# Kernel optimization log

Measured on AMD Instinct MI355X. Metric: run time of the kernel, lower is better.

## Reference

```python
import jax, jax.numpy as jnp
import numpy as np

B, S, D = 2, 1024, 1024
N_HEADS = 16
R = 128
M = 8
N_NEURONS = 256


def group_gate(gate, n_basis):
    # gate: [B,S,N] -> [B,S,M], sum over consecutive groups, then normalize
    b, s, n = gate.shape
    gs = n // n_basis  # exact by construction (256/8)
    g = gate.reshape(b, s, n_basis, gs).sum(axis=-1)
    return g / (g.sum(axis=-1, keepdims=True) + 1e-8)


def feature_fn(x, neurons, weights):
    # x:[B,S,D], neurons:[M,D,R], weights:[B,S,M] -> h:[B,S,R]
    all_h = jnp.einsum('bsd,mdr->bsmr', x, neurons)
    return jnp.einsum('bsmr,bsm->bsr', all_h, weights)


def restore_fn(h, neurons, weights):
    # h:[B,S,R], neurons:[M,R,D], weights:[B,S,M] -> [B,S,D]
    pre = jnp.einsum('bsr,bsm->bsmr', h, weights)
    return jnp.einsum('bsmr,mrd->bsd', pre, neurons)


def setup_inputs() -> dict:
    key = jax.random.key(0)
    ks = jax.random.split(key, 9)
    sc = 0.02
    return {
        'x': jax.random.normal(ks[0], (B, S, D), jnp.float32),
        'qk_f': jax.random.normal(ks[1], (M, D, R), jnp.float32) * sc,
        'qk_r': jax.random.normal(ks[2], (M, R, D), jnp.float32) * sc,
        'v_f': jax.random.normal(ks[3], (M, D, R), jnp.float32) * sc,
        'v_r': jax.random.normal(ks[4], (M, R, D), jnp.float32) * sc,
        'Wg_q': jax.random.normal(ks[5], (D, N_NEURONS), jnp.float32) * sc,
        'Wg_k': jax.random.normal(ks[6], (D, N_NEURONS), jnp.float32) * sc,
        'Wg_v': jax.random.normal(ks[7], (D, N_NEURONS), jnp.float32) * sc,
        'W_O': jax.random.normal(ks[8], (D, D), jnp.float32) * sc,
    }


def reference(x, qk_f, qk_r, v_f, v_r, Wg_q, Wg_k, Wg_v, W_O):
    # Router gates (softmax over neuron dim), then grouped per basis
    g_Q = jax.nn.softmax(jnp.einsum('bsd,dn->bsn', x, Wg_q), axis=-1)
    g_K = jax.nn.softmax(jnp.einsum('bsd,dn->bsn', x, Wg_k), axis=-1)
    g_V = jax.nn.softmax(jnp.einsum('bsd,dn->bsn', x, Wg_v), axis=-1)
    gQ_b = group_gate(g_Q, M)
    gK_b = group_gate(g_K, M)
    gV_b = group_gate(g_V, M)

    Q = restore_fn(feature_fn(x, qk_f, gQ_b), qk_r, gQ_b)
    K = restore_fn(feature_fn(x, qk_f, gK_b), qk_r, gK_b)
    V = restore_fn(feature_fn(x, v_f, gV_b), v_r, gV_b)

    d_head = D // N_HEADS
    Q = Q.reshape(B, S, N_HEADS, d_head).transpose(0, 2, 1, 3)
    K = K.reshape(B, S, N_HEADS, d_head).transpose(0, 2, 1, 3)
    V = V.reshape(B, S, N_HEADS, d_head).transpose(0, 2, 1, 3)

    scale = jnp.sqrt(jnp.float32(d_head))
    scores = jnp.einsum('bhsd,bhtd->bhst', Q, K) / scale
    causal = jnp.tril(jnp.ones((S, S), dtype=jnp.bool_))
    scores = jnp.where(causal, scores, jnp.finfo(scores.dtype).min)
    attn_w = jax.nn.softmax(scores, axis=-1)
    out = jnp.einsum('bhst,bhtd->bhsd', attn_w, V)
    out = out.transpose(0, 2, 1, 3).reshape(B, S, D)
    out = jnp.einsum('bsd,de->bse', out, W_O)
    return out
```

## Files before the change

### kernel.cpp

```cpp
#include <hip/hip_runtime.h>
#include <hip/hip_bf16.h>

#define BB 2
#define SS 1024
#define DD 1024
#define NH 16
#define DH 64
#define MM 8
#define RR 128
#define NN 256
#define NT (BB*SS)

using bf16 = __hip_bfloat16;

typedef __attribute__((ext_vector_type(8))) short short8;
typedef __attribute__((ext_vector_type(4))) short short4v;
typedef __attribute__((ext_vector_type(4))) float f32x4;

#define EXP2F(x) __builtin_amdgcn_exp2f(x)

#define GLD16(g, l) __builtin_amdgcn_global_load_lds( \
    (const __attribute__((address_space(1))) void*)(g), \
    (__attribute__((address_space(3))) void*)(l), 16, 0, 0)

__device__ __forceinline__ short8 lds_load8(const short* p) {
    short4v a = *(const short4v*)p;
    short4v b = *(const short4v*)(p + 4);
    short8 r;
    r[0] = a[0]; r[1] = a[1]; r[2] = a[2]; r[3] = a[3];
    r[4] = b[0]; r[5] = b[1]; r[6] = b[2]; r[7] = b[3];
    return r;
}

template <int NR>
__device__ __forceinline__ void stage_tile(const bf16* __restrict__ src, int k0,
                                           bf16* lds, int wave, int lane) {
#pragma unroll
    for (int i = 0; i < NR / 32; ++i) {
        const int L = i * 256 + wave * 64 + lane;
        const int row = L >> 3;
        const int gch = (L & 7) ^ ((row >> 1) & 7);
        GLD16(src + (size_t)row * DD + k0 + gch * 8, &lds[(i * 256 + wave * 64) * 8]);
    }
}

__device__ __forceinline__ short8 fragld(const bf16* lds, int rc, int kk, int quad) {
    int slot = (kk * 4 + quad) ^ ((rc >> 1) & 7);
    return *(const short8*)&((const short*)lds)[(rc * 8 + slot) * 8];
}

__device__ __forceinline__ void gemm64_std(
    const bf16* __restrict__ A, const bf16* __restrict__ Bt, bf16* __restrict__ C,
    int Nz, int m0, int n0, bf16* As, bf16* Bs,
    int wave, int lane, int quad, int l15) {
    const int wr = wave >> 1, wc = wave & 1;
    f32x4 acc[2][4];
#pragma unroll
    for (int i = 0; i < 2; ++i)
#pragma unroll
        for (int j = 0; j < 4; ++j) acc[i][j] = (f32x4)0.f;

    const bf16* Ab = A + (size_t)m0 * DD;
    const bf16* Bb = Bt + (size_t)n0 * DD;
    for (int k0 = 0; k0 < DD; k0 += 64) {
        __syncthreads();
        stage_tile<64>(Ab, k0, As, wave, lane);
        stage_tile<128>(Bb, k0, Bs, wave, lane);
        __syncthreads();
#pragma unroll
        for (int kk = 0; kk < 2; ++kk) {
            short8 aF[2], bF[4];
#pragma unroll
            for (int bi = 0; bi < 2; ++bi) aF[bi] = fragld(As, wr * 32 + bi * 16 + l15, kk, quad);
#pragma unroll
            for (int bj = 0; bj < 4; ++bj) bF[bj] = fragld(Bs, wc * 64 + bj * 16 + l15, kk, quad);
#pragma unroll
            for (int bi = 0; bi < 2; ++bi)
#pragma unroll
                for (int bj = 0; bj < 4; ++bj)
                    acc[bi][bj] = __builtin_amdgcn_mfma_f32_16x16x32_bf16(aF[bi], bF[bj], acc[bi][bj], 0, 0, 0);
        }
    }
#pragma unroll
    for (int bi = 0; bi < 2; ++bi)
#pragma unroll
        for (int bj = 0; bj < 4; ++bj)
#pragma unroll
            for (int r = 0; r < 4; ++r) {
                int row = m0 + wr * 32 + bi * 16 + quad * 4 + r;
                int col = n0 + wc * 64 + bj * 16 + l15;
                C[(size_t)row * Nz + col] = __float2bfloat16(acc[bi][bj][r]);
            }
}

__device__ __forceinline__ void gemm64_dualB(
    const bf16* __restrict__ A, const bf16* __restrict__ B0, const bf16* __restrict__ B1,
    bf16* __restrict__ C0, bf16* __restrict__ C1,
    int m0, int n0, bf16* As, bf16* Bs0, bf16* Bs1,
    int wave, int lane, int quad, int l15) {
    const int wr = wave >> 1, wc = wave & 1;
    f32x4 acc0[2][4], acc1[2][4];
#pragma unroll
    for (int i = 0; i < 2; ++i)
#pragma unroll
        for (int j = 0; j < 4; ++j) { acc0[i][j] = (f32x4)0.f; acc1[i][j] = (f32x4)0.f; }

    const bf16* Ab  = A  + (size_t)m0 * DD;
    const bf16* B0b = B0 + (size_t)n0 * DD;
    const bf16* B1b = B1 + (size_t)n0 * DD;
    for (int k0 = 0; k0 < DD; k0 += 64) {
        __syncthreads();
        stage_tile<64>(Ab, k0, As, wave, lane);
        stage_tile<128>(B0b, k0, Bs0, wave, lane);
        stage_tile<128>(B1b, k0, Bs1, wave, lane);
        __syncthreads();
#pragma unroll
        for (int kk = 0; kk < 2; ++kk) {
            short8 aF[2], bF[4];
#pragma unroll
            for (int bi = 0; bi < 2; ++bi) aF[bi] = fragld(As, wr * 32 + bi * 16 + l15, kk, quad);
#pragma unroll
            for (int bj = 0; bj < 4; ++bj) bF[bj] = fragld(Bs0, wc * 64 + bj * 16 + l15, kk, quad);
#pragma unroll
            for (int bi = 0; bi < 2; ++bi)
#pragma unroll
                for (int bj = 0; bj < 4; ++bj)
                    acc0[bi][bj] = __builtin_amdgcn_mfma_f32_16x16x32_bf16(aF[bi], bF[bj], acc0[bi][bj], 0, 0, 0);
#pragma unroll
            for (int bj = 0; bj < 4; ++bj) bF[bj] = fragld(Bs1, wc * 64 + bj * 16 + l15, kk, quad);
#pragma unroll
            for (int bi = 0; bi < 2; ++bi)
#pragma unroll
                for (int bj = 0; bj < 4; ++bj)
                    acc1[bi][bj] = __builtin_amdgcn_mfma_f32_16x16x32_bf16(aF[bi], bF[bj], acc1[bi][bj], 0, 0, 0);
        }
    }
#pragma unroll
    for (int bi = 0; bi < 2; ++bi)
#pragma unroll
        for (int bj = 0; bj < 4; ++bj)
#pragma unroll
            for (int r = 0; r < 4; ++r) {
                int row = m0 + wr * 32 + bi * 16 + quad * 4 + r;
                int col = n0 + wc * 64 + bj * 16 + l15;
                C0[(size_t)row * DD + col] = __float2bfloat16(acc0[bi][bj][r]);
                C1[(size_t)row * DD + col] = __float2bfloat16(acc1[bi][bj][r]);
            }
}

__device__ __forceinline__ void gemm64_dualA(
    const bf16* __restrict__ A0, const bf16* __restrict__ A1, const bf16* __restrict__ Bt,
    bf16* __restrict__ C0, bf16* __restrict__ C1,
    int m0, int n0, bf16* As0, bf16* As1, bf16* Bs,
    int wave, int lane, int quad, int l15) {
    const int wr = wave >> 1, wc = wave & 1;
    f32x4 acc0[2][4], acc1[2][4];
#pragma unroll
    for (int i = 0; i < 2; ++i)
#pragma unroll
        for (int j = 0; j < 4; ++j) { acc0[i][j] = (f32x4)0.f; acc1[i][j] = (f32x4)0.f; }

    const bf16* A0b = A0 + (size_t)m0 * DD;
    const bf16* A1b = A1 + (size_t)m0 * DD;
    const bf16* Bb  = Bt + (size_t)n0 * DD;
    for (int k0 = 0; k0 < DD; k0 += 64) {
        __syncthreads();
        stage_tile<64>(A0b, k0, As0, wave, lane);
        stage_tile<64>(A1b, k0, As1, wave, lane);
        stage_tile<128>(Bb, k0, Bs, wave, lane);
        __syncthreads();
#pragma unroll
        for (int kk = 0; kk < 2; ++kk) {
            short8 aF0[2], aF1[2], bF[4];
#pragma unroll
            for (int bi = 0; bi < 2; ++bi) {
                aF0[bi] = fragld(As0, wr * 32 + bi * 16 + l15, kk, quad);
                aF1[bi] = fragld(As1, wr * 32 + bi * 16 + l15, kk, quad);
            }
#pragma unroll
            for (int bj = 0; bj < 4; ++bj) bF[bj] = fragld(Bs, wc * 64 + bj * 16 + l15, kk, quad);
#pragma unroll
            for (int bi = 0; bi < 2; ++bi)
#pragma unroll
                for (int bj = 0; bj < 4; ++bj)
                    acc0[bi][bj] = __builtin_amdgcn_mfma_f32_16x16x32_bf16(aF0[bi], bF[bj], acc0[bi][bj], 0, 0, 0);
#pragma unroll
            for (int bi = 0; bi < 2; ++bi)
#pragma unroll
                for (int bj = 0; bj < 4; ++bj)
                    acc1[bi][bj] = __builtin_amdgcn_mfma_f32_16x16x32_bf16(aF1[bi], bF[bj], acc1[bi][bj], 0, 0, 0);
        }
    }
#pragma unroll
    for (int bi = 0; bi < 2; ++bi)
#pragma unroll
        for (int bj = 0; bj < 4; ++bj)
#pragma unroll
            for (int r = 0; r < 4; ++r) {
                int row = m0 + wr * 32 + bi * 16 + quad * 4 + r;
                int col = n0 + wc * 64 + bj * 16 + l15;
                C0[(size_t)row * DD + col] = __float2bfloat16(acc0[bi][bj][r]);
                C1[(size_t)row * DD + col] = __float2bfloat16(acc1[bi][bj][r]);
            }
}

struct ProjArgs {
    const bf16 *xb, *f0, *f1, *wg;
    bf16 *allh0, *allh1, *lg;
    const float* csrc[3];
    bf16* cdst[3];
};

__global__ __launch_bounds__(256, 3) void mfma_proj(ProjArgs P) {
    __shared__ __align__(16) char smem[40960];
    const int bidx = blockIdx.x;
    const int tid = threadIdx.x;

    if (bidx >= 448) {
        float (*tile)[33] = (float(*)[33])smem;
        const int cb = bidx - 448;
        const int j = cb >> 10;
        const int t = cb & 1023;
        const int kb = t >> 5, rb = t & 31;
        const int tx = tid & 31, ty0 = tid >> 5;
        const float* s = P.csrc[j] + ((size_t)(kb * 32) * 1024) + rb * 32 + tx;
#pragma unroll
        for (int p = 0; p < 4; ++p)
            tile[ty0 + p * 8][tx] = s[(size_t)(ty0 + p * 8) * 1024];
        __syncthreads();
        bf16* dd = P.cdst[j] + ((size_t)(rb * 32) * 1024) + kb * 32 + tx;
#pragma unroll
        for (int p = 0; p < 4; ++p)
            dd[(size_t)(ty0 + p * 8) * 1024] = __float2bfloat16(tile[tx][ty0 + p * 8]);
        return;
    }

    bf16* As  = (bf16*)smem;
    bf16* Bs0 = As + 64 * 64;
    bf16* Bs1 = Bs0 + 128 * 64;
    const int wave = tid >> 6, lane = tid & 63;
    const int quad = lane >> 4, l15 = lane & 15;
    const int wk = (bidx & 7) * 56 + (bidx >> 3);
    if (wk < 256) {
        const int m0 = (wk >> 3) * 64, n0 = (wk & 7) * 128;
        gemm64_dualB(P.xb, P.f0, P.f1, P.allh0, P.allh1, m0, n0,
                     As, Bs0, Bs1, wave, lane, quad, l15);
    } else {
        const int r = wk - 256;
        const int m0 = (r / 6) * 64, n0 = (r % 6) * 128;
        gemm64_std(P.xb, P.wg, P.lg, 768, m0, n0, As, Bs0, wave, lane, quad, l15);
    }
}

struct RestArgs {
    const bf16 *preQ, *preK, *preV, *qkr, *vr;
    bf16 *Qb, *Kb, *Vb;
};

__global__ __launch_bounds__(256, 3) void mfma_restore(RestArgs R) {
    __shared__ __align__(16) char smem[32768];
    bf16* As0 = (bf16*)smem;
    bf16* As1 = As0 + 64 * 64;
    bf16* Bs  = As1 + 64 * 64;
    const int tid = threadIdx.x;
    const int wave = tid >> 6, lane = tid & 63;
    const int quad = lane >> 4, l15 = lane & 15;
    const int wk = (blockIdx.x & 7) * 64 + (blockIdx.x >> 3);
    if (wk < 256) {
        const int m0 = (wk >> 3) * 64, n0 = (wk & 7) * 128;
        gemm64_dualA(R.preQ, R.preK, R.qkr, R.Qb, R.Kb, m0, n0,
                     As0, As1, Bs, wave, lane, quad, l15);
    } else {
        const int r = wk - 256;
        const int m0 = (r >> 3) * 64, n0 = (r & 7) * 128;
        gemm64_std(R.preV, R.vr, R.Vb, DD, m0, n0, As0, Bs, wave, lane, quad, l15);
    }
}

__global__ __launch_bounds__(256) void mfma_wo(
    const bf16* __restrict__ A, const bf16* __restrict__ Bt, float* __restrict__ C) {
    __shared__ __align__(16) bf16 As[64 * 64];
    __shared__ __align__(16) bf16 Bs[64 * 64];
    const int tid = threadIdx.x;
    const int wave = tid >> 6, lane = tid & 63;
    const int quad = lane >> 4, l15 = lane & 15;
    const int wr = wave >> 1, wc = wave & 1;
    const int wk = (blockIdx.x & 7) * 64 + (blockIdx.x >> 3);
    const int m0 = (wk >> 4) * 64, n0 = (wk & 15) * 64;

    f32x4 acc[2][2];
#pragma unroll
    for (int i = 0; i < 2; ++i)
#pragma unroll
        for (int j = 0; j < 2; ++j) acc[i][j] = (f32x4)0.f;

    const bf16* Ab = A + (size_t)m0 * DD;
    const bf16* Bb = Bt + (size_t)n0 * DD;
    for (int k0 = 0; k0 < DD; k0 += 64) {
        __syncthreads();
        stage_tile<64>(Ab, k0, As, wave, lane);
        stage_tile<64>(Bb, k0, Bs, wave, lane);
        __syncthreads();
#pragma unroll
        for (int kk = 0; kk < 2; ++kk) {
            short8 aF[2], bF[2];
#pragma unroll
            for (int bi = 0; bi < 2; ++bi) aF[bi] = fragld(As, wr * 32 + bi * 16 + l15, kk, quad);
#pragma unroll
            for (int bj = 0; bj < 2; ++bj) bF[bj] = fragld(Bs, wc * 32 + bj * 16 + l15, kk, quad);
#pragma unroll
            for (int bi = 0; bi < 2; ++bi)
#pragma unroll
                for (int bj = 0; bj < 2; ++bj)
                    acc[bi][bj] = __builtin_amdgcn_mfma_f32_16x16x32_bf16(aF[bi], bF[bj], acc[bi][bj], 0, 0, 0);
        }
    }
#pragma unroll
    for (int bi = 0; bi < 2; ++bi)
#pragma unroll
        for (int bj = 0; bj < 2; ++bj)
#pragma unroll
            for (int r = 0; r < 4; ++r) {
                int row = m0 + wr * 32 + bi * 16 + quad * 4 + r;
                int col = n0 + wc * 32 + bj * 16 + l15;
                C[(size_t)row * DD + col] = acc[bi][bj][r];
            }
}

struct ConvJobs {
    const float* src[9];
    bf16* dst[9];
    int K[9], R[9], G[9];
    int tEnd[9];
};

__global__ void convert_kernel(ConvJobs J) {
    __shared__ float tile[32][33];
    const int b = blockIdx.x;
    int j = 0;
    while (j < 8 && b >= J.tEnd[j]) ++j;
    const int local = b - (j > 0 ? J.tEnd[j - 1] : 0);
    const float* src = J.src[j];
    bf16* dst = J.dst[j];
    const int tid = threadIdx.x;

    if (J.G[j] == 0) {
        size_t base = (size_t)local * 4096 + (size_t)tid * 16;
        const float4* s4 = (const float4*)(src + base);
        short* d = (short*)(dst + base);
#pragma unroll
        for (int c = 0; c < 4; ++c) {
            float4 v = s4[c];
            short4v o;
            bf16 t0 = __float2bfloat16(v.x); o[0] = *(short*)&t0;
            bf16 t1 = __float2bfloat16(v.y); o[1] = *(short*)&t1;
            bf16 t2 = __float2bfloat16(v.z); o[2] = *(short*)&t2;
            bf16 t3 = __float2bfloat16(v.w); o[3] = *(short*)&t3;
            *(short4v*)(d + c * 4) = o;
        }
    } else {
        const int Kj = J.K[j], Rj = J.R[j];
        const int Rb = Rj >> 5, Kb = Kj >> 5;
        const int perG = Kb * Rb;
        const int g = local / perG;
        const int rem = local - g * perG;
        const int kb = rem / Rb, rb = rem - kb * Rb;
        const int tx = tid & 31, ty0 = tid >> 5;
        const float* s = src + ((size_t)(g * Kj + kb * 32) * Rj) + rb * 32 + tx;
#pragma unroll
        for (int p = 0; p < 4; ++p)
            tile[ty0 + p * 8][tx] = s[(size_t)(ty0 + p * 8) * Rj];
        __syncthreads();
        bf16* dd = dst + ((size_t)(g * Rj + rb * 32) * Kj) + kb * 32 + tx;
#pragma unroll
        for (int p = 0; p < 4; ++p)
            dd[(size_t)(ty0 + p * 8) * Kj] = __float2bfloat16(tile[tx][ty0 + p * 8]);
    }
}

__global__ void gate_combine(const bf16* __restrict__ logitsAll,
                             const bf16* __restrict__ allh,
                             bf16* __restrict__ preQ, bf16* __restrict__ preK,
                             bf16* __restrict__ preV) {
    const int t = blockIdx.x;
    const int n = threadIdx.x;
    const int wave = n >> 6, lane = n & 63;
    __shared__ float wred[3][4];
    __shared__ float sred[3][4];
    __shared__ float gred[3][8];

    float v[3], e[3];
#pragma unroll
    for (int z = 0; z < 3; ++z)
        v[z] = __bfloat162float(logitsAll[(size_t)t * 768 + z * 256 + n]);

    float mz[3];
#pragma unroll
    for (int z = 0; z < 3; ++z) {
        mz[z] = v[z];
#pragma unroll
        for (int off = 1; off <= 32; off <<= 1)
            mz[z] = fmaxf(mz[z], __shfl_xor(mz[z], off));
    }
    if (lane == 0) {
#pragma unroll
        for (int z = 0; z < 3; ++z) wred[z][wave] = mz[z];
    }
    __syncthreads();
    float gmax[3];
#pragma unroll
    for (int z = 0; z < 3; ++z)
        gmax[z] = fmaxf(fmaxf(wred[z][0], wred[z][1]), fmaxf(wred[z][2], wred[z][3]));

    float ws[3];
#pragma unroll
    for (int z = 0; z < 3; ++z) {
        e[z] = __expf(v[z] - gmax[z]);
        ws[z] = e[z];
#pragma unroll
        for (int off = 1; off <= 32; off <<= 1)
            ws[z] += __shfl_xor(ws[z], off);
    }
    if (lane == 0) {
#pragma unroll
        for (int z = 0; z < 3; ++z) sred[z][wave] = ws[z];
    }
    float gs[3];
#pragma unroll
    for (int z = 0; z < 3; ++z) {
        gs[z] = e[z];
#pragma unroll
        for (int off = 1; off <= 16; off <<= 1)
            gs[z] += __shfl_xor(gs[z], off);
    }
    __syncthreads();
    float total[3];
#pragma unroll
    for (int z = 0; z < 3; ++z)
        total[z] = sred[z][0] + sred[z][1] + sred[z][2] + sred[z][3];
    if ((n & 31) == 0) {
#pragma unroll
        for (int z = 0; z < 3; ++z) gred[z][n >> 5] = gs[z] / total[z];
    }
    __syncthreads();

    float gv[3][8];
#pragma unroll
    for (int z = 0; z < 3; ++z) {
        float tot = 0.f;
#pragma unroll
        for (int m = 0; m < 8; ++m) tot += gred[z][m];
        float inv = 1.0f / (tot + 1e-8f);
#pragma unroll
        for (int m = 0; m < 8; ++m) gv[z][m] = gred[z][m] * inv;
    }

    const int r0 = n & 127;
    const int half = n >> 7;
    const bf16* src_qk = allh + (size_t)t * 1024;
    const bf16* src_v  = allh + (size_t)NT * DD + (size_t)t * 1024;
    float hq = 0.f, hk = 0.f, hv = 0.f;
#pragma unroll
    for (int m = 0; m < 8; ++m) {
        float aqk = __bfloat162float(src_qk[m * 128 + r0]);
        float av  = __bfloat162float(src_v[m * 128 + r0]);
        hq += aqk * gv[0][m];
        hk += aqk * gv[1][m];
        hv += av  * gv[2][m];
    }
    __syncthreads();
#pragma unroll
    for (int mm = 0; mm < 4; ++mm) {
        int m = half * 4 + mm;
        size_t o = (size_t)t * 1024 + m * 128 + r0;
        preQ[o] = __float2bfloat16(hq * gv[0][m]);
        preK[o] = __float2bfloat16(hk * gv[1][m]);
        preV[o] = __float2bfloat16(hv * gv[2][m]);
    }
}

#define LDK 68

__global__ __launch_bounds__(256) void flash_attn_causal(
    const bf16* __restrict__ Q, const bf16* __restrict__ K,
    const bf16* __restrict__ V, bf16* __restrict__ out) {
    const int bx = blockIdx.x;
    const int xcd = bx & 7, slot = bx >> 3;
    const int bh = xcd * 4 + (slot & 3);
    const int qtk = slot >> 2;
    const int qt = (qtk < 8) ? (15 - qtk) : (qtk - 8);
    const int b = bh >> 4;
    const int h = bh & 15;
    const int kt_hi = qt + 1;

    const int tid = threadIdx.x;
    const int wave = tid >> 6;
    const int lane = tid & 63;
    const int quad = lane >> 4;
    const int l15 = lane & 15;

    __shared__ short Ks[2][64 * 64];
    __shared__ short Vt[2][64 * LDK];
    __shared__ short Ps[4 * 16 * LDK];

    const int q_row = qt * 64 + wave * 16 + l15;
    const bf16* qptr = Q + (size_t)(b * SS + q_row) * DD + h * DH + quad * 8;
    short8 aq0 = *(const short8*)qptr;
    short8 aq1 = *(const short8*)(qptr + 32);

    const int krp = tid & 31;
    const int dhb = (tid >> 5) * 8;

    float m_r[4], l_r[4];
    f32x4 o[4];
#pragma unroll
    for (int r = 0; r < 4; ++r) { m_r[r] = -3.0e38f; l_r[r] = 0.f; }
#pragma unroll
    for (int cc = 0; cc < 4; ++cc) o[cc] = (f32x4)0.f;

    const float SCL2 = 0.18033688f;

    {
#pragma unroll
        for (int i = 0; i < 2; ++i) {
            const int L = i * 256 + wave * 64 + lane;
            const int row = L >> 3;
            const int gch = (L & 7) ^ ((row >> 1) & 7);
            GLD16(K + (size_t)(b * SS + row) * DD + h * DH + gch * 8,
                  &Ks[0][(i * 256 + wave * 64) * 8]);
        }
        const bf16* s0 = V + (size_t)(b * SS + 2 * krp) * DD + h * DH + dhb;
        short8 r0 = *(const short8*)s0;
        short8 r1 = *(const short8*)(s0 + DD);
#pragma unroll
        for (int i = 0; i < 8; ++i) {
            unsigned int pk = (unsigned short)r0[i] | ((unsigned int)(unsigned short)r1[i] << 16);
            *(unsigned int*)&Vt[0][(dhb + i) * LDK + 2 * krp] = pk;
        }
        __syncthreads();
    }

    for (int kt = 0; kt < kt_hi; ++kt) {
        const int buf = kt & 1;
        const bool pf = (kt + 1 < kt_hi);
        short8 pr0, pr1;
        if (pf) {
#pragma unroll
            for (int i = 0; i < 2; ++i) {
                const int L = i * 256 + wave * 64 + lane;
                const int row = L >> 3;
                const int gch = (L & 7) ^ ((row >> 1) & 7);
                GLD16(K + (size_t)(b * SS + (kt + 1) * 64 + row) * DD + h * DH + gch * 8,
                      &Ks[buf ^ 1][(i * 256 + wave * 64) * 8]);
            }
            const bf16* s0 = V + (size_t)(b * SS + (kt + 1) * 64 + 2 * krp) * DD + h * DH + dhb;
            pr0 = *(const short8*)s0;
            pr1 = *(const short8*)(s0 + DD);
        }

        const short* KsB = Ks[buf];
        f32x4 s[4];
#pragma unroll
        for (int cc = 0; cc < 4; ++cc) {
            int n = cc * 16 + l15;
            int sl0 = quad ^ ((n >> 1) & 7);
            int sl1 = (quad + 4) ^ ((n >> 1) & 7);
            short8 bk0 = *(const short8*)&KsB[(n * 8 + sl0) * 8];
            short8 bk1 = *(const short8*)&KsB[(n * 8 + sl1) * 8];
            f32x4 acc = (f32x4)0.f;
            acc = __builtin_amdgcn_mfma_f32_16x16x32_bf16(aq0, bk0, acc, 0, 0, 0);
            acc = __builtin_amdgcn_mfma_f32_16x16x32_bf16(aq1, bk1, acc, 0, 0, 0);
            s[cc] = acc;
        }

        const bool diag = (kt == qt);
#pragma unroll
        for (int cc = 0; cc < 4; ++cc) {
#pragma unroll
            for (int r = 0; r < 4; ++r) {
                float v = s[cc][r] * SCL2;
                if (diag) {
                    int row_rel = wave * 16 + quad * 4 + r;
                    int col_rel = cc * 16 + l15;
                    if (col_rel > row_rel) v = -3.0e38f;
                }
                s[cc][r] = v;
            }
        }

        float mx[4];
#pragma unroll
        for (int r = 0; r < 4; ++r) {
            float m2 = fmaxf(fmaxf(s[0][r], s[1][r]), fmaxf(s[2][r], s[3][r]));
            m2 = fmaxf(m2, __shfl_xor(m2, 1));
            m2 = fmaxf(m2, __shfl_xor(m2, 2));
            m2 = fmaxf(m2, __shfl_xor(m2, 4));
            m2 = fmaxf(m2, __shfl_xor(m2, 8));
            mx[r] = m2;
        }
        bool grew = false;
#pragma unroll
        for (int r = 0; r < 4; ++r) grew = grew || (mx[r] > m_r[r] + 8.f);
        float alpha[4];
        const bool need = __any(grew);
        if (need) {
#pragma unroll
            for (int r = 0; r < 4; ++r) {
                float nm = fmaxf(m_r[r], mx[r]);
                alpha[r] = EXP2F(m_r[r] - nm);
                m_r[r] = nm;
            }
        }

        float p[4][4];
#pragma unroll
        for (int r = 0; r < 4; ++r) {
            float rs = 0.f;
#pragma unroll
            for (int cc = 0; cc < 4; ++cc) {
                float e = EXP2F(s[cc][r] - m_r[r]);
                p[cc][r] = e;
                rs += e;
            }
            rs += __shfl_xor(rs, 1);
            rs += __shfl_xor(rs, 2);
            rs += __shfl_xor(rs, 4);
            rs += __shfl_xor(rs, 8);
            if (need) l_r[r] = l_r[r] * alpha[r] + rs;
            else      l_r[r] += rs;
        }
        if (need) {
#pragma unroll
            for (int cc = 0; cc < 4; ++cc)
#pragma unroll
                for (int r = 0; r < 4; ++r) o[cc][r] *= alpha[r];
        }

        short* pw = &Ps[wave * 16 * LDK];
#pragma unroll
        for (int cc = 0; cc < 4; ++cc)
#pragma unroll
            for (int r = 0; r < 4; ++r) {
                bf16 hb = __float2bfloat16(p[cc][r]);
                pw[(quad * 4 + r) * LDK + cc * 16 + l15] = *(short*)&hb;
            }

        short8 ap0 = lds_load8(&pw[l15 * LDK + quad * 8]);
        short8 ap1 = lds_load8(&pw[l15 * LDK + 32 + quad * 8]);

        const short* VtB = Vt[buf];
#pragma unroll
        for (int cc = 0; cc < 4; ++cc) {
            short8 bv0 = lds_load8(&VtB[(cc * 16 + l15) * LDK + quad * 8]);
            short8 bv1 = lds_load8(&VtB[(cc * 16 + l15) * LDK + 32 + quad * 8]);
            o[cc] = __builtin_amdgcn_mfma_f32_16x16x32_bf16(ap0, bv0, o[cc], 0, 0, 0);
            o[cc] = __builtin_amdgcn_mfma_f32_16x16x32_bf16(ap1, bv1, o[cc], 0, 0, 0);
        }

        if (pf) {
#pragma unroll
            for (int i = 0; i < 8; ++i) {
                unsigned int pk = (unsigned short)pr0[i] | ((unsigned int)(unsigned short)pr1[i] << 16);
                *(unsigned int*)&Vt[buf ^ 1][(dhb + i) * LDK + 2 * krp] = pk;
            }
        }
        __syncthreads();
    }

    float inv[4];
#pragma unroll
    for (int r = 0; r < 4; ++r) inv[r] = 1.0f / l_r[r];
#pragma unroll
    for (int cc = 0; cc < 4; ++cc)
#pragma unroll
        for (int r = 0; r < 4; ++r) {
            int row = qt * 64 + wave * 16 + quad * 4 + r;
            out[(size_t)(b * SS + row) * DD + h * DH + cc * 16 + l15] =
                __float2bfloat16(o[cc][r] * inv[r]);
        }
}

extern "C" void kernel_launch(void* const* d_in, const int* in_sizes, int n_in,
                              void* d_out, int out_size, void* d_ws, size_t ws_size,
                              hipStream_t stream) {
    const float* x    = (const float*)d_in[0];
    const float* qk_f = (const float*)d_in[1];
    const float* qk_r = (const float*)d_in[2];
    const float* v_f  = (const float*)d_in[3];
    const float* v_r  = (const float*)d_in[4];
    const float* Wg_q = (const float*)d_in[5];
    const float* Wg_k = (const float*)d_in[6];
    const float* Wg_v = (const float*)d_in[7];
    const float* W_O  = (const float*)d_in[8];

    char* w = (char*)d_ws;
    const size_t MB = 1 << 20;
    bf16* xb     = (bf16*)(w + 0);
    bf16* wg_bt  = (bf16*)(w + 4 * MB);
    bf16* fbt    = (bf16*)(w + (size_t)(5.5 * MB));
    bf16* logits = (bf16*)(w + (size_t)(9.5 * MB));
    bf16* qkr_bt = (bf16*)(w + 16 * MB);
    bf16* vr_bt  = (bf16*)(w + 18 * MB);
    bf16* wo_bt  = (bf16*)(w + 20 * MB);
    bf16* preQ   = (bf16*)(w + 0);
    bf16* preK   = (bf16*)(w + 4 * MB);
    bf16* Kb     = (bf16*)(w + 8 * MB);
    bf16* Vb     = (bf16*)(w + 12 * MB);
    bf16* attnb  = (bf16*)(w + 0);
    bf16* allh   = (bf16*)d_out;
    bf16* preV   = allh + (size_t)NT * DD;
    bf16* Qb     = (bf16*)d_out;
    float* out   = (float*)d_out;

    ConvJobs J;
    J.src[0] = x;    J.dst[0] = xb;               J.K[0] = 0;    J.R[0] = 0;    J.G[0] = 0;
    J.src[1] = qk_f; J.dst[1] = fbt;              J.K[1] = 1024; J.R[1] = 128;  J.G[1] = 8;
    J.src[2] = v_f;  J.dst[2] = fbt + 1024*1024;  J.K[2] = 1024; J.R[2] = 128;  J.G[2] = 8;
    J.src[3] = Wg_q; J.dst[3] = wg_bt;            J.K[3] = 1024; J.R[3] = 256;  J.G[3] = 1;
    J.src[4] = Wg_k; J.dst[4] = wg_bt + 256*1024; J.K[4] = 1024; J.R[4] = 256;  J.G[4] = 1;
    J.src[5] = Wg_v; J.dst[5] = wg_bt + 2*256*1024; J.K[5] = 1024; J.R[5] = 256; J.G[5] = 1;
    int tiles[6] = {512, 1024, 1024, 256, 256, 256};
    int cum = 0;
    for (int i = 0; i < 6; ++i) { cum += tiles[i]; J.tEnd[i] = cum; }
    for (int i = 6; i < 9; ++i) { J.tEnd[i] = cum; J.src[i] = nullptr; J.dst[i] = nullptr; J.K[i] = J.R[i] = J.G[i] = 0; }
    convert_kernel<<<cum, 256, 0, stream>>>(J);

    ProjArgs Pp;
    Pp.xb = xb; Pp.f0 = fbt; Pp.f1 = fbt + 1024*1024; Pp.wg = wg_bt;
    Pp.allh0 = allh; Pp.allh1 = allh + (size_t)NT * DD; Pp.lg = logits;
    Pp.csrc[0] = qk_r; Pp.csrc[1] = v_r; Pp.csrc[2] = W_O;
    Pp.cdst[0] = qkr_bt; Pp.cdst[1] = vr_bt; Pp.cdst[2] = wo_bt;
    mfma_proj<<<dim3(3520), 256, 0, stream>>>(Pp);

    gate_combine<<<NT, 256, 0, stream>>>(logits, allh, preQ, preK, preV);

    RestArgs Pr;
    Pr.preQ = preQ; Pr.preK = preK; Pr.preV = preV;
    Pr.qkr = qkr_bt; Pr.vr = vr_bt;
    Pr.Qb = Qb; Pr.Kb = Kb; Pr.Vb = Vb;
    mfma_restore<<<dim3(512), 256, 0, stream>>>(Pr);

    flash_attn_causal<<<dim3(512), 256, 0, stream>>>(Qb, Kb, Vb, attnb);

    mfma_wo<<<dim3(512), 256, 0, stream>>>(attnb, wo_bt, out);
}
```

Before: 193.2 us.

## Double-buffer LDS tiles in GEMMs and split dual-operand blocks into independent tiles

Adds double-buffered LDS staging to the projection, restore and output GEMMs, so the next k-tile's async global-to-LDS loads are issued while MFMA runs on the current tile. This drops one barrier per iteration. It also removes the dual-A and dual-B fused GEMM variants, which shared one operand across two outputs, and launches more single-output blocks instead (proj 3520→3776, restore 512→768). The cost is twice the LDS per block, which may lower occupancy, and the shared operand is now loaded twice.

```diff
diff --git a/kernel.cpp b/kernel.cpp
--- a/kernel.cpp
+++ b/kernel.cpp
@@ -49,7 +49,7 @@
     return *(const short8*)&((const short*)lds)[(rc * 8 + slot) * 8];
 }
 
-__device__ __forceinline__ void gemm64_std(
+__device__ __forceinline__ void gemm64_pipe(
     const bf16* __restrict__ A, const bf16* __restrict__ Bt, bf16* __restrict__ C,
     int Nz, int m0, int n0, bf16* As, bf16* Bs,
     int wave, int lane, int quad, int l15) {
@@ -62,25 +62,35 @@
 
     const bf16* Ab = A + (size_t)m0 * DD;
     const bf16* Bb = Bt + (size_t)n0 * DD;
+
+    stage_tile<64>(Ab, 0, As, wave, lane);
+    stage_tile<128>(Bb, 0, Bs, wave, lane);
+    __syncthreads();
+
     for (int k0 = 0; k0 < DD; k0 += 64) {
-        __syncthreads();
-        stage_tile<64>(Ab, k0, As, wave, lane);
-        stage_tile<128>(Bb, k0, Bs, wave, lane);
-        __syncthreads();
+        const int buf = (k0 >> 6) & 1;
+        const bf16* Asc = As + buf * (64 * 64);
+        const bf16* Bsc = Bs + buf * (128 * 64);
+        if (k0 + 64 < DD) {
+            stage_tile<64>(Ab, k0 + 64, As + (buf ^ 1) * (64 * 64), wave, lane);
+            stage_tile<128>(Bb, k0 + 64, Bs + (buf ^ 1) * (128 * 64), wave, lane);
+        }
 #pragma unroll
         for (int kk = 0; kk < 2; ++kk) {
             short8 aF[2], bF[4];
 #pragma unroll
-            for (int bi = 0; bi < 2; ++bi) aF[bi] = fragld(As, wr * 32 + bi * 16 + l15, kk, quad);
-#pragma unroll
-            for (int bj = 0; bj < 4; ++bj) bF[bj] = fragld(Bs, wc * 64 + bj * 16 + l15, kk, quad);
+            for (int bi = 0; bi < 2; ++bi) aF[bi] = fragld(Asc, wr * 32 + bi * 16 + l15, kk, quad);
+#pragma unroll
+            for (int bj = 0; bj < 4; ++bj) bF[bj] = fragld(Bsc, wc * 64 + bj * 16 + l15, kk, quad);
 #pragma unroll
             for (int bi = 0; bi < 2; ++bi)
 #pragma unroll
                 for (int bj = 0; bj < 4; ++bj)
                     acc[bi][bj] = __builtin_amdgcn_mfma_f32_16x16x32_bf16(aF[bi], bF[bj], acc[bi][bj], 0, 0, 0);
         }
-    }
+        __syncthreads();
+    }
+
 #pragma unroll
     for (int bi = 0; bi < 2; ++bi)
 #pragma unroll
@@ -90,117 +100,6 @@
                 int row = m0 + wr * 32 + bi * 16 + quad * 4 + r;
                 int col = n0 + wc * 64 + bj * 16 + l15;
                 C[(size_t)row * Nz + col] = __float2bfloat16(acc[bi][bj][r]);
-            }
-}
-
-__device__ __forceinline__ void gemm64_dualB(
-    const bf16* __restrict__ A, const bf16* __restrict__ B0, const bf16* __restrict__ B1,
-    bf16* __restrict__ C0, bf16* __restrict__ C1,
-    int m0, int n0, bf16* As, bf16* Bs0, bf16* Bs1,
-    int wave, int lane, int quad, int l15) {
-    const int wr = wave >> 1, wc = wave & 1;
-    f32x4 acc0[2][4], acc1[2][4];
-#pragma unroll
-    for (int i = 0; i < 2; ++i)
-#pragma unroll
-        for (int j = 0; j < 4; ++j) { acc0[i][j] = (f32x4)0.f; acc1[i][j] = (f32x4)0.f; }
-
-    const bf16* Ab  = A  + (size_t)m0 * DD;
-    const bf16* B0b = B0 + (size_t)n0 * DD;
-    const bf16* B1b = B1 + (size_t)n0 * DD;
-    for (int k0 = 0; k0 < DD; k0 += 64) {
-        __syncthreads();
-        stage_tile<64>(Ab, k0, As, wave, lane);
-        stage_tile<128>(B0b, k0, Bs0, wave, lane);
-        stage_tile<128>(B1b, k0, Bs1, wave, lane);
-        __syncthreads();
-#pragma unroll
-        for (int kk = 0; kk < 2; ++kk) {
-            short8 aF[2], bF[4];
-#pragma unroll
-            for (int bi = 0; bi < 2; ++bi) aF[bi] = fragld(As, wr * 32 + bi * 16 + l15, kk, quad);
-#pragma unroll
-            for (int bj = 0; bj < 4; ++bj) bF[bj] = fragld(Bs0, wc * 64 + bj * 16 + l15, kk, quad);
-#pragma unroll
-            for (int bi = 0; bi < 2; ++bi)
-#pragma unroll
-                for (int bj = 0; bj < 4; ++bj)
-                    acc0[bi][bj] = __builtin_amdgcn_mfma_f32_16x16x32_bf16(aF[bi], bF[bj], acc0[bi][bj], 0, 0, 0);
-#pragma unroll
-            for (int bj = 0; bj < 4; ++bj) bF[bj] = fragld(Bs1, wc * 64 + bj * 16 + l15, kk, quad);
-#pragma unroll
-            for (int bi = 0; bi < 2; ++bi)
-#pragma unroll
-                for (int bj = 0; bj < 4; ++bj)
-                    acc1[bi][bj] = __builtin_amdgcn_mfma_f32_16x16x32_bf16(aF[bi], bF[bj], acc1[bi][bj], 0, 0, 0);
-        }
-    }
-#pragma unroll
-    for (int bi = 0; bi < 2; ++bi)
-#pragma unroll
-        for (int bj = 0; bj < 4; ++bj)
-#pragma unroll
-            for (int r = 0; r < 4; ++r) {
-                int row = m0 + wr * 32 + bi * 16 + quad * 4 + r;
-                int col = n0 + wc * 64 + bj * 16 + l15;
-                C0[(size_t)row * DD + col] = __float2bfloat16(acc0[bi][bj][r]);
-                C1[(size_t)row * DD + col] = __float2bfloat16(acc1[bi][bj][r]);
-            }
-}
-
-__device__ __forceinline__ void gemm64_dualA(
-    const bf16* __restrict__ A0, const bf16* __restrict__ A1, const bf16* __restrict__ Bt,
-    bf16* __restrict__ C0, bf16* __restrict__ C1,
-    int m0, int n0, bf16* As0, bf16* As1, bf16* Bs,
-    int wave, int lane, int quad, int l15) {
-    const int wr = wave >> 1, wc = wave & 1;
-    f32x4 acc0[2][4], acc1[2][4];
-#pragma unroll
-    for (int i = 0; i < 2; ++i)
-#pragma unroll
-        for (int j = 0; j < 4; ++j) { acc0[i][j] = (f32x4)0.f; acc1[i][j] = (f32x4)0.f; }
-
-    const bf16* A0b = A0 + (size_t)m0 * DD;
-    const bf16* A1b = A1 + (size_t)m0 * DD;
-    const bf16* Bb  = Bt + (size_t)n0 * DD;
-    for (int k0 = 0; k0 < DD; k0 += 64) {
-        __syncthreads();
-        stage_tile<64>(A0b, k0, As0, wave, lane);
-        stage_tile<64>(A1b, k0, As1, wave, lane);
-        stage_tile<128>(Bb, k0, Bs, wave, lane);
-        __syncthreads();
-#pragma unroll
-        for (int kk = 0; kk < 2; ++kk) {
-            short8 aF0[2], aF1[2], bF[4];
-#pragma unroll
-            for (int bi = 0; bi < 2; ++bi) {
-                aF0[bi] = fragld(As0, wr * 32 + bi * 16 + l15, kk, quad);
-                aF1[bi] = fragld(As1, wr * 32 + bi * 16 + l15, kk, quad);
-            }
-#pragma unroll
-            for (int bj = 0; bj < 4; ++bj) bF[bj] = fragld(Bs, wc * 64 + bj * 16 + l15, kk, quad);
-#pragma unroll
-            for (int bi = 0; bi < 2; ++bi)
-#pragma unroll
-                for (int bj = 0; bj < 4; ++bj)
-                    acc0[bi][bj] = __builtin_amdgcn_mfma_f32_16x16x32_bf16(aF0[bi], bF[bj], acc0[bi][bj], 0, 0, 0);
-#pragma unroll
-            for (int bi = 0; bi < 2; ++bi)
-#pragma unroll
-                for (int bj = 0; bj < 4; ++bj)
-                    acc1[bi][bj] = __builtin_amdgcn_mfma_f32_16x16x32_bf16(aF1[bi], bF[bj], acc1[bi][bj], 0, 0, 0);
-        }
-    }
-#pragma unroll
-    for (int bi = 0; bi < 2; ++bi)
-#pragma unroll
-        for (int bj = 0; bj < 4; ++bj)
-#pragma unroll
-            for (int r = 0; r < 4; ++r) {
-                int row = m0 + wr * 32 + bi * 16 + quad * 4 + r;
-                int col = n0 + wc * 64 + bj * 16 + l15;
-                C0[(size_t)row * DD + col] = __float2bfloat16(acc0[bi][bj][r]);
-                C1[(size_t)row * DD + col] = __float2bfloat16(acc1[bi][bj][r]);
             }
 }
 
@@ -212,13 +111,13 @@
 };
 
 __global__ __launch_bounds__(256, 3) void mfma_proj(ProjArgs P) {
-    __shared__ __align__(16) char smem[40960];
+    __shared__ __align__(16) char smem[49152];
     const int bidx = blockIdx.x;
     const int tid = threadIdx.x;
 
-    if (bidx >= 448) {
+    if (bidx >= 704) {
         float (*tile)[33] = (float(*)[33])smem;
-        const int cb = bidx - 448;
+        const int cb = bidx - 704;
         const int j = cb >> 10;
         const int t = cb & 1023;
         const int kb = t >> 5, rb = t & 31;
@@ -235,52 +134,47 @@
         return;
     }
 
-    bf16* As  = (bf16*)smem;
-    bf16* Bs0 = As + 64 * 64;
-    bf16* Bs1 = Bs0 + 128 * 64;
+    bf16* As = (bf16*)smem;
+    bf16* Bs = As + 2 * 64 * 64;
     const int wave = tid >> 6, lane = tid & 63;
     const int quad = lane >> 4, l15 = lane & 15;
-    const int wk = (bidx & 7) * 56 + (bidx >> 3);
-    if (wk < 256) {
-        const int m0 = (wk >> 3) * 64, n0 = (wk & 7) * 128;
-        gemm64_dualB(P.xb, P.f0, P.f1, P.allh0, P.allh1, m0, n0,
-                     As, Bs0, Bs1, wave, lane, quad, l15);
+    const int wk = (bidx & 7) * 88 + (bidx >> 3);
+    if (wk < 512) {
+        const int z = wk >> 8;
+        const int r = wk & 255;
+        gemm64_pipe(P.xb, z ? P.f1 : P.f0, z ? P.allh1 : P.allh0, 1024,
+                    (r >> 3) * 64, (r & 7) * 128, As, Bs, wave, lane, quad, l15);
     } else {
-        const int r = wk - 256;
-        const int m0 = (r / 6) * 64, n0 = (r % 6) * 128;
-        gemm64_std(P.xb, P.wg, P.lg, 768, m0, n0, As, Bs0, wave, lane, quad, l15);
-    }
-}
-
-struct RestArgs {
-    const bf16 *preQ, *preK, *preV, *qkr, *vr;
-    bf16 *Qb, *Kb, *Vb;
+        const int r = wk - 512;
+        gemm64_pipe(P.xb, P.wg, P.lg, 768, (r / 6) * 64, (r % 6) * 128,
+                    As, Bs, wave, lane, quad, l15);
+    }
+}
+
+struct RestZ {
+    const bf16* A[3];
+    const bf16* Bt[3];
+    bf16* C[3];
 };
 
-__global__ __launch_bounds__(256, 3) void mfma_restore(RestArgs R) {
-    __shared__ __align__(16) char smem[32768];
-    bf16* As0 = (bf16*)smem;
-    bf16* As1 = As0 + 64 * 64;
-    bf16* Bs  = As1 + 64 * 64;
+__global__ __launch_bounds__(256, 3) void mfma_restore(RestZ R) {
+    __shared__ __align__(16) char smem[49152];
+    bf16* As = (bf16*)smem;
+    bf16* Bs = As + 2 * 64 * 64;
     const int tid = threadIdx.x;
     const int wave = tid >> 6, lane = tid & 63;
     const int quad = lane >> 4, l15 = lane & 15;
-    const int wk = (blockIdx.x & 7) * 64 + (blockIdx.x >> 3);
-    if (wk < 256) {
-        const int m0 = (wk >> 3) * 64, n0 = (wk & 7) * 128;
-        gemm64_dualA(R.preQ, R.preK, R.qkr, R.Qb, R.Kb, m0, n0,
-                     As0, As1, Bs, wave, lane, quad, l15);
-    } else {
-        const int r = wk - 256;
-        const int m0 = (r >> 3) * 64, n0 = (r & 7) * 128;
-        gemm64_std(R.preV, R.vr, R.Vb, DD, m0, n0, As0, Bs, wave, lane, quad, l15);
-    }
-}
-
-__global__ __launch_bounds__(256) void mfma_wo(
+    const int wk = (blockIdx.x & 7) * 96 + (blockIdx.x >> 3);
+    const int z = wk >> 8;
+    const int r = wk & 255;
+    gemm64_pipe(R.A[z], R.Bt[z], R.C[z], DD, (r >> 3) * 64, (r & 7) * 128,
+                As, Bs, wave, lane, quad, l15);
+}
+
+__global__ __launch_bounds__(256, 4) void mfma_wo(
     const bf16* __restrict__ A, const bf16* __restrict__ Bt, float* __restrict__ C) {
-    __shared__ __align__(16) bf16 As[64 * 64];
-    __shared__ __align__(16) bf16 Bs[64 * 64];
+    __shared__ __align__(16) bf16 As[2 * 64 * 64];
+    __shared__ __align__(16) bf16 Bs[2 * 64 * 64];
     const int tid = threadIdx.x;
     const int wave = tid >> 6, lane = tid & 63;
     const int quad = lane >> 4, l15 = lane & 15;
@@ -296,24 +190,33 @@
 
     const bf16* Ab = A + (size_t)m0 * DD;
     const bf16* Bb = Bt + (size_t)n0 * DD;
+
+    stage_tile<64>(Ab, 0, As, wave, lane);
+    stage_tile<64>(Bb, 0, Bs, wave, lane);
+    __syncthreads();
+
     for (int k0 = 0; k0 < DD; k0 += 64) {
-        __syncthreads();
-        stage_tile<64>(Ab, k0, As, wave, lane);
-        stage_tile<64>(Bb, k0, Bs, wave, lane);
-        __syncthreads();
+        const int buf = (k0 >> 6) & 1;
+        const bf16* Asc = As + buf * (64 * 64);
+        const bf16* Bsc = Bs + buf * (64 * 64);
+        if (k0 + 64 < DD) {
+            stage_tile<64>(Ab, k0 + 64, As + (buf ^ 1) * (64 * 64), wave, lane);
+            stage_tile<64>(Bb, k0 + 64, Bs + (buf ^ 1) * (64 * 64), wave, lane);
+        }
 #pragma unroll
         for (int kk = 0; kk < 2; ++kk) {
             short8 aF[2], bF[2];
 #pragma unroll
-            for (int bi = 0; bi < 2; ++bi) aF[bi] = fragld(As, wr * 32 + bi * 16 + l15, kk, quad);
-#pragma unroll
-            for (int bj = 0; bj < 2; ++bj) bF[bj] = fragld(Bs, wc * 32 + bj * 16 + l15, kk, quad);
+            for (int bi = 0; bi < 2; ++bi) aF[bi] = fragld(Asc, wr * 32 + bi * 16 + l15, kk, quad);
+#pragma unroll
+            for (int bj = 0; bj < 2; ++bj) bF[bj] = fragld(Bsc, wc * 32 + bj * 16 + l15, kk, quad);
 #pragma unroll
             for (int bi = 0; bi < 2; ++bi)
 #pragma unroll
                 for (int bj = 0; bj < 2; ++bj)
                     acc[bi][bj] = __builtin_amdgcn_mfma_f32_16x16x32_bf16(aF[bi], bF[bj], acc[bi][bj], 0, 0, 0);
         }
+        __syncthreads();
     }
 #pragma unroll
     for (int bi = 0; bi < 2; ++bi)
@@ -730,15 +633,15 @@
     Pp.allh0 = allh; Pp.allh1 = allh + (size_t)NT * DD; Pp.lg = logits;
     Pp.csrc[0] = qk_r; Pp.csrc[1] = v_r; Pp.csrc[2] = W_O;
     Pp.cdst[0] = qkr_bt; Pp.cdst[1] = vr_bt; Pp.cdst[2] = wo_bt;
-    mfma_proj<<<dim3(3520), 256, 0, stream>>>(Pp);
+    mfma_proj<<<dim3(3776), 256, 0, stream>>>(Pp);
 
     gate_combine<<<NT, 256, 0, stream>>>(logits, allh, preQ, preK, preV);
 
-    RestArgs Pr;
-    Pr.preQ = preQ; Pr.preK = preK; Pr.preV = preV;
-    Pr.qkr = qkr_bt; Pr.vr = vr_bt;
-    Pr.Qb = Qb; Pr.Kb = Kb; Pr.Vb = Vb;
-    mfma_restore<<<dim3(512), 256, 0, stream>>>(Pr);
+    RestZ Pr;
+    Pr.A[0] = preQ; Pr.A[1] = preK; Pr.A[2] = preV;
+    Pr.Bt[0] = qkr_bt; Pr.Bt[1] = qkr_bt; Pr.Bt[2] = vr_bt;
+    Pr.C[0] = Qb; Pr.C[1] = Kb; Pr.C[2] = Vb;
+    mfma_restore<<<dim3(768), 256, 0, stream>>>(Pr);
 
     flash_attn_causal<<<dim3(512), 256, 0, stream>>>(Qb, Kb, Vb, attnb);
 
```

New measurement: 186.7 us. 3.4% less time.
